# Kernel tuning notes

Measured on AMD Instinct MI355X. Metric: run time of the kernel, lower is better.

Reference implementation:

```python
import jax, jax.numpy as jnp
import numpy as np

N = 10000
E = 640000
IN_CH = 512
OUT_CH = 256
K = 2


def setup_inputs() -> dict:
    key = jax.random.key(0)
    k1, k2, k3, k4, k5 = jax.random.split(key, 5)
    x = jax.random.normal(k1, (N, IN_CH), dtype=jnp.float32)
    edge_index = jax.random.randint(k2, (2, E), 0, N, dtype=jnp.int64)
    lin_w = jax.random.normal(k3, (OUT_CH, IN_CH), dtype=jnp.float32) * (1.0 / np.sqrt(IN_CH))
    lin_b = jax.random.normal(k4, (OUT_CH,), dtype=jnp.float32) * 0.01
    weights = jax.random.uniform(k5, (K,), dtype=jnp.float32)
    return {"x": x, "edge_index": edge_index, "lin_w": lin_w, "lin_b": lin_b, "weights": weights}


def reference(x, edge_index, lin_w, lin_b, weights):
    n = x.shape[0]
    row, col = edge_index[0], edge_index[1]
    # deg = bincount(row); symmetric-normalized edge weights
    deg = jax.ops.segment_sum(jnp.ones(row.shape[0], dtype=x.dtype), row, num_segments=n)
    deg_inv_sqrt = jnp.where(deg > 0, jax.lax.rsqrt(deg), 0.0)
    norm = deg_inv_sqrt[row] * deg_inv_sqrt[col]  # [E]

    def spmm(h):
        # y[i] = sum_{e: row[e]==i} norm[e] * h[col[e]]
        return jax.ops.segment_sum(norm[:, None] * h[col], row, num_segments=n)

    out = x @ lin_w.T + lin_b  # [N, OUT_CH]
    # Faithful ARMA loop: x_k starts from the CURRENT accumulated `out` each hop-group
    for k in range(K):
        x_k = out
        for _ in range(k + 1):
            x_k = spmm(x_k)
        out = out + weights[k] * x_k
    return out
```

## Files before the change

kernel.cpp:

```cpp
#include <hip/hip_runtime.h>

#define N_NODES 10000
#define E_EDGES 640000
#define IN_CH   512
#define OUT_CH  256
#define HALF_CH 128
#define CSR_CAP (E_EDGES + 16 * N_NODES + 128)
#define G_GEMM_X 157
#define G_GEMM  (G_GEMM_X * 2)
#define HBLK    125
#define EPB     5120

typedef short bf16x8 __attribute__((ext_vector_type(8)));
typedef float f32x4  __attribute__((ext_vector_type(4)));

__device__ __forceinline__ unsigned short f2b(float f) {
    unsigned int u = __float_as_uint(f);
    return (unsigned short)((u + 0x7FFFu + ((u >> 16) & 1u)) >> 16);
}
__device__ __forceinline__ float lo16(unsigned int u) { return __uint_as_float(u << 16); }
__device__ __forceinline__ float hi16(unsigned int u) { return __uint_as_float(u & 0xFFFF0000u); }
__device__ __forceinline__ float b2f(unsigned short u) { return __uint_as_float(((unsigned int)u) << 16); }

__global__ __launch_bounds__(256) void hist_rank(const int* __restrict__ row,
                                                 int* __restrict__ cnt,
                                                 unsigned short* __restrict__ rank) {
    __shared__ int hist[N_NODES];
    int b = blockIdx.x, tid = threadIdx.x;
    for (int i = tid; i < N_NODES; i += 256) hist[i] = 0;
    __syncthreads();
    int ebase = b * EPB;
    #pragma unroll 4
    for (int i = tid; i < EPB; i += 256) {
        int r = row[ebase + i];
        rank[ebase + i] = (unsigned short)atomicAdd(&hist[r], 1);
    }
    __syncthreads();
    int* cb = cnt + (size_t)b * N_NODES;
    for (int i = tid; i < N_NODES; i += 256) cb[i] = hist[i];
}

__global__ void alloc2(int* __restrict__ cnt,
                       int2* __restrict__ seg,
                       float* __restrict__ dinv, float* __restrict__ sq,
                       int* __restrict__ counter, int* __restrict__ csr_col, int n) {
    int r = blockIdx.x * blockDim.x + threadIdx.x;
    if (r >= n) return;
    int d = 0;
    for (int b = 0; b < HBLK; b++) d += cnt[(size_t)b * N_NODES + r];
    dinv[r] = (d > 0) ? rsqrtf((float)d) : 0.0f;
    sq[r]   = (d > 0) ? sqrtf((float)d) : 0.0f;
    int pad = (d + 15) & ~15;
    int s = atomicAdd(counter, pad);
    seg[r] = make_int2(s, s + pad);
    int run = s;
    for (int b = 0; b < HBLK; b++) {
        int c = cnt[(size_t)b * N_NODES + r];
        cnt[(size_t)b * N_NODES + r] = run;
        run += c;
    }
    for (int j = d; j < pad; j++) csr_col[s + j] = N_NODES;
}

__global__ __launch_bounds__(256) void gemm_scatter(const float* __restrict__ x,
                                                    const float* __restrict__ w,
                                                    const float* __restrict__ bias,
                                                    const float* __restrict__ dinv,
                                                    unsigned short* __restrict__ h0b,
                                                    const int* __restrict__ row,
                                                    const int* __restrict__ col,
                                                    const int* __restrict__ base,
                                                    const unsigned short* __restrict__ rank,
                                                    int* __restrict__ csr_col) {
    __shared__ unsigned short As[64][72];
    __shared__ unsigned short Bs[128][72];
    int bid = blockIdx.x;
    int tid = threadIdx.x;
    if (bid >= G_GEMM) {
        int sb = bid - G_GEMM;
        const int* bb = base + (size_t)sb * N_NODES;
        int ebase = sb * EPB;
        #pragma unroll 4
        for (int i = tid; i < EPB; i += 256) {
            int e = ebase + i;
            int r = row[e];
            int p = bb[r] + (int)rank[e];
            csr_col[p] = col[e];
        }
        return;
    }
    int bx = bid % G_GEMM_X;
    int plane = bid / G_GEMM_X;
    int wave = tid >> 6, lane = tid & 63, quad = lane >> 4, l16 = lane & 15;
    int row0 = bx * 64;
    int n0 = plane * 128;
    unsigned short* h0b_p = h0b + (size_t)plane * (N_NODES + 1) * HALF_CH;

    int ar = tid >> 2;
    int aseg = (tid & 3) * 16;
    int br = tid >> 1;
    int bseg = (tid & 1) * 32;

    f32x4 acc[8] = {};
    for (int k0 = 0; k0 < IN_CH; k0 += 64) {
        {
            int gr = row0 + ar;
            if (gr < N_NODES) {
                const float4* src = (const float4*)(x + (size_t)gr * IN_CH + k0 + aseg);
                #pragma unroll
                for (int i = 0; i < 4; i++) {
                    float4 v = src[i];
                    ushort4 o;
                    o.x = f2b(v.x); o.y = f2b(v.y); o.z = f2b(v.z); o.w = f2b(v.w);
                    *(ushort4*)&As[ar][aseg + i * 4] = o;
                }
            } else {
                ushort4 z = {0, 0, 0, 0};
                #pragma unroll
                for (int i = 0; i < 4; i++) *(ushort4*)&As[ar][aseg + i * 4] = z;
            }
        }
        {
            const float4* src = (const float4*)(w + (size_t)(n0 + br) * IN_CH + k0 + bseg);
            #pragma unroll
            for (int i = 0; i < 8; i++) {
                float4 v = src[i];
                ushort4 o;
                o.x = f2b(v.x); o.y = f2b(v.y); o.z = f2b(v.z); o.w = f2b(v.w);
                *(ushort4*)&Bs[br][bseg + i * 4] = o;
            }
        }
        __syncthreads();
        #pragma unroll
        for (int kk = 0; kk < 2; kk++) {
            bf16x8 a = *(const bf16x8*)&As[wave * 16 + l16][kk * 32 + quad * 8];
            #pragma unroll
            for (int t = 0; t < 8; t++) {
                bf16x8 b = *(const bf16x8*)&Bs[t * 16 + l16][kk * 32 + quad * 8];
                acc[t] = __builtin_amdgcn_mfma_f32_16x16x32_bf16(a, b, acc[t], 0, 0, 0);
            }
        }
        __syncthreads();
    }
    #pragma unroll
    for (int t = 0; t < 8; t++) {
        int lcol = t * 16 + l16;
        int col_ = n0 + lcol;
        float bv = bias[col_];
        #pragma unroll
        for (int r = 0; r < 4; r++) {
            int grow = row0 + wave * 16 + quad * 4 + r;
            if (grow < N_NODES) {
                float v = acc[t][r] + bv;
                h0b_p[(size_t)grow * HALF_CH + lcol] = f2b(v * dinv[grow]);
            }
        }
    }
    if (bx == 0 && tid < 64)
        ((unsigned int*)(h0b_p + (size_t)N_NODES * HALF_CH))[tid] = 0u;
}

__global__ __launch_bounds__(256) void spmm_kernel(const unsigned short* __restrict__ hb,
                                                   const int2* __restrict__ seg,
                                                   const int* __restrict__ csr_col,
                                                   const float* __restrict__ dinv,
                                                   const float* __restrict__ sq,
                                                   const unsigned short* __restrict__ prev_b,
                                                   const float* __restrict__ wts, int widx,
                                                   unsigned short* __restrict__ yb_out,
                                                   float* __restrict__ axpy_out,
                                                   unsigned short* __restrict__ axpyb_out,
                                                   int n) {
    int plane = blockIdx.x & 1;
    int node = (blockIdx.x >> 1) * 4 + (threadIdx.x >> 6);
    int lane = threadIdx.x & 63;
    if (node >= n) return;
    int sub = lane >> 4, l16 = lane & 15;
    size_t pstride = (size_t)(n + 1) * HALF_CH;
    const unsigned short* hp = hb + (size_t)plane * pstride;

    int2 se = seg[node];
    int s = se.x, e = se.y;
    float acc[8] = {0.f, 0.f, 0.f, 0.f, 0.f, 0.f, 0.f, 0.f};
    if (s < e) {
        int c0 = csr_col[s + 0  + sub];
        int c1 = csr_col[s + 4  + sub];
        int c2 = csr_col[s + 8  + sub];
        int c3 = csr_col[s + 12 + sub];
        int p = s;
        while (true) {
            int pn = p + 16;
            int n0c = csr_col[pn + 0  + sub];
            int n1c = csr_col[pn + 4  + sub];
            int n2c = csr_col[pn + 8  + sub];
            int n3c = csr_col[pn + 12 + sub];
            uint4 v0 = *(const uint4*)(hp + (size_t)c0 * HALF_CH + l16 * 8);
            uint4 v1 = *(const uint4*)(hp + (size_t)c1 * HALF_CH + l16 * 8);
            uint4 v2 = *(const uint4*)(hp + (size_t)c2 * HALF_CH + l16 * 8);
            uint4 v3 = *(const uint4*)(hp + (size_t)c3 * HALF_CH + l16 * 8);
            acc[0] += lo16(v0.x) + lo16(v1.x) + lo16(v2.x) + lo16(v3.x);
            acc[1] += hi16(v0.x) + hi16(v1.x) + hi16(v2.x) + hi16(v3.x);
            acc[2] += lo16(v0.y) + lo16(v1.y) + lo16(v2.y) + lo16(v3.y);
            acc[3] += hi16(v0.y) + hi16(v1.y) + hi16(v2.y) + hi16(v3.y);
            acc[4] += lo16(v0.z) + lo16(v1.z) + lo16(v2.z) + lo16(v3.z);
            acc[5] += hi16(v0.z) + hi16(v1.z) + hi16(v2.z) + hi16(v3.z);
            acc[6] += lo16(v0.w) + lo16(v1.w) + lo16(v2.w) + lo16(v3.w);
            acc[7] += hi16(v0.w) + hi16(v1.w) + hi16(v2.w) + hi16(v3.w);
            c0 = n0c; c1 = n1c; c2 = n2c; c3 = n3c; p = pn;
            if (p >= e) break;
        }
    }
    #pragma unroll
    for (int k = 0; k < 8; k++) {
        acc[k] += __shfl_xor(acc[k], 16, 64);
        acc[k] += __shfl_xor(acc[k], 32, 64);
    }
    if (sub != 0) return;

    float di = dinv[node];
    float y[8];
    #pragma unroll
    for (int k = 0; k < 8; k++) y[k] = di * acc[k];

    size_t pbase = (size_t)plane * pstride + (size_t)node * HALF_CH + l16 * 8;
    size_t padrow = (size_t)plane * pstride + (size_t)n * HALF_CH + l16 * 8;
    if (yb_out) {
        ushort4 o0, o1;
        o0.x = f2b(di * y[0]); o0.y = f2b(di * y[1]); o0.z = f2b(di * y[2]); o0.w = f2b(di * y[3]);
        o1.x = f2b(di * y[4]); o1.y = f2b(di * y[5]); o1.z = f2b(di * y[6]); o1.w = f2b(di * y[7]);
        *(ushort4*)(yb_out + pbase) = o0;
        *(ushort4*)(yb_out + pbase + 4) = o1;
        if (node == 0) {
            ushort4 z = {0, 0, 0, 0};
            *(ushort4*)(yb_out + padrow) = z;
            *(ushort4*)(yb_out + padrow + 4) = z;
        }
    }
    if (prev_b) {
        float wk = wts[widx];
        float sqn = sq[node];
        ushort4 p0 = *(const ushort4*)(prev_b + pbase);
        ushort4 p1 = *(const ushort4*)(prev_b + pbase + 4);
        float o[8];
        o[0] = b2f(p0.x) * sqn + wk * y[0];
        o[1] = b2f(p0.y) * sqn + wk * y[1];
        o[2] = b2f(p0.z) * sqn + wk * y[2];
        o[3] = b2f(p0.w) * sqn + wk * y[3];
        o[4] = b2f(p1.x) * sqn + wk * y[4];
        o[5] = b2f(p1.y) * sqn + wk * y[5];
        o[6] = b2f(p1.z) * sqn + wk * y[6];
        o[7] = b2f(p1.w) * sqn + wk * y[7];
        if (axpy_out) {
            size_t fbase = (size_t)node * OUT_CH + plane * HALF_CH + l16 * 8;
            float4 f0 = {o[0], o[1], o[2], o[3]};
            float4 f1 = {o[4], o[5], o[6], o[7]};
            *(float4*)(axpy_out + fbase) = f0;
            *(float4*)(axpy_out + fbase + 4) = f1;
        }
        if (axpyb_out) {
            ushort4 b0, b1;
            b0.x = f2b(di * o[0]); b0.y = f2b(di * o[1]); b0.z = f2b(di * o[2]); b0.w = f2b(di * o[3]);
            b1.x = f2b(di * o[4]); b1.y = f2b(di * o[5]); b1.z = f2b(di * o[6]); b1.w = f2b(di * o[7]);
            *(ushort4*)(axpyb_out + pbase) = b0;
            *(ushort4*)(axpyb_out + pbase + 4) = b1;
            if (node == 0) {
                ushort4 z = {0, 0, 0, 0};
                *(ushort4*)(axpyb_out + padrow) = z;
                *(ushort4*)(axpyb_out + padrow + 4) = z;
            }
        }
    }
}

extern "C" void kernel_launch(void* const* d_in, const int* in_sizes, int n_in,
                              void* d_out, int out_size, void* d_ws, size_t ws_size,
                              hipStream_t stream) {
    const float* x     = (const float*)d_in[0];
    const int*   ei    = (const int*)d_in[1];
    const float* lin_w = (const float*)d_in[2];
    const float* lin_b = (const float*)d_in[3];
    const float* wts   = (const float*)d_in[4];
    float* out = (float*)d_out;

    char* ws = (char*)d_ws;
    size_t off = 0;
    auto alloc = [&](size_t bytes) -> void* {
        void* p = ws + off;
        off += (bytes + 255) & ~(size_t)255;
        return p;
    };
    int*   cnt      = (int*)  alloc((size_t)HBLK * N_NODES * 4);
    unsigned short* rank = (unsigned short*)alloc((size_t)E_EDGES * 2);
    int*   counter  = (int*)  alloc(256);
    int2*  seg      = (int2*) alloc((size_t)N_NODES * 8);
    float* dinv     = (float*)alloc(N_NODES * 4);
    float* sq       = (float*)alloc(N_NODES * 4);
    int*   csr_col  = (int*)  alloc((size_t)CSR_CAP * 4);
    unsigned short* h0b   = (unsigned short*)alloc((size_t)2 * (N_NODES + 1) * HALF_CH * 2);
    unsigned short* out1b = (unsigned short*)alloc((size_t)2 * (N_NODES + 1) * HALF_CH * 2);
    unsigned short* t2b   = (unsigned short*)alloc((size_t)2 * (N_NODES + 1) * HALF_CH * 2);

    hipMemsetAsync(counter, 0, 4, stream);

    const int* row = ei;
    const int* col = ei + E_EDGES;

    hist_rank<<<HBLK, 256, 0, stream>>>(row, cnt, rank);
    alloc2<<<(N_NODES + 255) / 256, 256, 0, stream>>>(cnt, seg, dinv, sq,
                                                      counter, csr_col, N_NODES);

    gemm_scatter<<<G_GEMM + HBLK, 256, 0, stream>>>(x, lin_w, lin_b, dinv, h0b,
                                                    row, col, cnt, rank, csr_col);

    int sgrid = 2 * ((N_NODES + 3) / 4);
    spmm_kernel<<<sgrid, 256, 0, stream>>>(h0b, seg, csr_col, dinv, sq, h0b,
                                           wts, 0, nullptr, nullptr, out1b, N_NODES);
    spmm_kernel<<<sgrid, 256, 0, stream>>>(out1b, seg, csr_col, dinv, sq, nullptr,
                                           wts, 0, t2b, nullptr, nullptr, N_NODES);
    spmm_kernel<<<sgrid, 256, 0, stream>>>(t2b, seg, csr_col, dinv, sq, out1b,
                                           wts, 1, nullptr, out, nullptr, N_NODES);
}
```

Baseline: 200.2 us.

## Transpose histogram count layout, parallelize CSR allocation per wave, widen SpMM gather unroll

Histogram counts are stored node-major (node × 128 blocks) instead of block-major, so the allocation kernel gives one wave per node and computes the per-block offsets with a wave-level prefix scan instead of a serial 125-iteration loop per thread. CSR segment padding goes from 16 to 32 entries, and the SpMM inner loop gathers 8 neighbor rows per lane per iteration instead of 4, giving more memory-level parallelism. The cost is more padded dummy edges, which are wasted gathers for low-degree nodes, higher register pressure, and strided scattered stores in hist_rank.

```diff
diff --git a/kernel.cpp b/kernel.cpp
--- a/kernel.cpp
+++ b/kernel.cpp
@@ -5,11 +5,12 @@
 #define IN_CH   512
 #define OUT_CH  256
 #define HALF_CH 128
-#define CSR_CAP (E_EDGES + 16 * N_NODES + 128)
+#define CSR_CAP (E_EDGES + 32 * N_NODES + 256)
 #define G_GEMM_X 157
 #define G_GEMM  (G_GEMM_X * 2)
 #define HBLK    125
 #define EPB     5120
+#define CNT_LD  128
 
 typedef short bf16x8 __attribute__((ext_vector_type(8)));
 typedef float f32x4  __attribute__((ext_vector_type(4)));
@@ -36,30 +37,42 @@
         rank[ebase + i] = (unsigned short)atomicAdd(&hist[r], 1);
     }
     __syncthreads();
-    int* cb = cnt + (size_t)b * N_NODES;
-    for (int i = tid; i < N_NODES; i += 256) cb[i] = hist[i];
-}
-
-__global__ void alloc2(int* __restrict__ cnt,
-                       int2* __restrict__ seg,
-                       float* __restrict__ dinv, float* __restrict__ sq,
-                       int* __restrict__ counter, int* __restrict__ csr_col, int n) {
-    int r = blockIdx.x * blockDim.x + threadIdx.x;
+    for (int i = tid; i < N_NODES; i += 256) cnt[(size_t)i * CNT_LD + b] = hist[i];
+}
+
+__global__ __launch_bounds__(256) void alloc2(int* __restrict__ cnt,
+                                              int2* __restrict__ seg,
+                                              float* __restrict__ dinv, float* __restrict__ sq,
+                                              int* __restrict__ counter,
+                                              int* __restrict__ csr_col, int n) {
+    int r = blockIdx.x * 4 + (threadIdx.x >> 6);
+    int lane = threadIdx.x & 63;
     if (r >= n) return;
-    int d = 0;
-    for (int b = 0; b < HBLK; b++) d += cnt[(size_t)b * N_NODES + r];
-    dinv[r] = (d > 0) ? rsqrtf((float)d) : 0.0f;
-    sq[r]   = (d > 0) ? sqrtf((float)d) : 0.0f;
-    int pad = (d + 15) & ~15;
-    int s = atomicAdd(counter, pad);
-    seg[r] = make_int2(s, s + pad);
-    int run = s;
-    for (int b = 0; b < HBLK; b++) {
-        int c = cnt[(size_t)b * N_NODES + r];
-        cnt[(size_t)b * N_NODES + r] = run;
-        run += c;
-    }
-    for (int j = d; j < pad; j++) csr_col[s + j] = N_NODES;
+    int* cr = cnt + (size_t)r * CNT_LD;
+    int v0 = cr[lane];
+    int v1 = (lane < HBLK - 64) ? cr[64 + lane] : 0;
+    int s0 = v0, s1 = v1;
+    #pragma unroll
+    for (int off = 1; off < 64; off <<= 1) {
+        int t0 = __shfl_up(s0, off, 64);
+        int t1 = __shfl_up(s1, off, 64);
+        if (lane >= off) { s0 += t0; s1 += t1; }
+    }
+    int tot0 = __shfl(s0, 63, 64);
+    int d = tot0 + __shfl(s1, 63, 64);
+    int pad = (d + 31) & ~31;
+    int s = 0;
+    if (lane == 0) s = atomicAdd(counter, pad);
+    s = __shfl(s, 0, 64);
+    if (lane == 0) {
+        dinv[r] = (d > 0) ? rsqrtf((float)d) : 0.0f;
+        sq[r]   = (d > 0) ? sqrtf((float)d) : 0.0f;
+        seg[r] = make_int2(s, s + pad);
+    }
+    cr[lane] = s + s0 - v0;
+    if (lane < HBLK - 64) cr[64 + lane] = s + tot0 + s1 - v1;
+    int j = d + lane;
+    if (j < pad) csr_col[s + j] = N_NODES;
 }
 
 __global__ __launch_bounds__(256) void gemm_scatter(const float* __restrict__ x,
@@ -78,13 +91,12 @@
     int tid = threadIdx.x;
     if (bid >= G_GEMM) {
         int sb = bid - G_GEMM;
-        const int* bb = base + (size_t)sb * N_NODES;
         int ebase = sb * EPB;
         #pragma unroll 4
         for (int i = tid; i < EPB; i += 256) {
             int e = ebase + i;
             int r = row[e];
-            int p = bb[r] + (int)rank[e];
+            int p = base[(size_t)r * CNT_LD + sb] + (int)rank[e];
             csr_col[p] = col[e];
         }
         return;
@@ -183,30 +195,29 @@
     int s = se.x, e = se.y;
     float acc[8] = {0.f, 0.f, 0.f, 0.f, 0.f, 0.f, 0.f, 0.f};
     if (s < e) {
-        int c0 = csr_col[s + 0  + sub];
-        int c1 = csr_col[s + 4  + sub];
-        int c2 = csr_col[s + 8  + sub];
-        int c3 = csr_col[s + 12 + sub];
+        int c[8];
+        #pragma unroll
+        for (int g = 0; g < 8; g++) c[g] = csr_col[s + 4 * g + sub];
         int p = s;
         while (true) {
-            int pn = p + 16;
-            int n0c = csr_col[pn + 0  + sub];
-            int n1c = csr_col[pn + 4  + sub];
-            int n2c = csr_col[pn + 8  + sub];
-            int n3c = csr_col[pn + 12 + sub];
-            uint4 v0 = *(const uint4*)(hp + (size_t)c0 * HALF_CH + l16 * 8);
-            uint4 v1 = *(const uint4*)(hp + (size_t)c1 * HALF_CH + l16 * 8);
-            uint4 v2 = *(const uint4*)(hp + (size_t)c2 * HALF_CH + l16 * 8);
-            uint4 v3 = *(const uint4*)(hp + (size_t)c3 * HALF_CH + l16 * 8);
-            acc[0] += lo16(v0.x) + lo16(v1.x) + lo16(v2.x) + lo16(v3.x);
-            acc[1] += hi16(v0.x) + hi16(v1.x) + hi16(v2.x) + hi16(v3.x);
-            acc[2] += lo16(v0.y) + lo16(v1.y) + lo16(v2.y) + lo16(v3.y);
-            acc[3] += hi16(v0.y) + hi16(v1.y) + hi16(v2.y) + hi16(v3.y);
-            acc[4] += lo16(v0.z) + lo16(v1.z) + lo16(v2.z) + lo16(v3.z);
-            acc[5] += hi16(v0.z) + hi16(v1.z) + hi16(v2.z) + hi16(v3.z);
-            acc[6] += lo16(v0.w) + lo16(v1.w) + lo16(v2.w) + lo16(v3.w);
-            acc[7] += hi16(v0.w) + hi16(v1.w) + hi16(v2.w) + hi16(v3.w);
-            c0 = n0c; c1 = n1c; c2 = n2c; c3 = n3c; p = pn;
+            int pn = p + 32;
+            int nc[8];
+            #pragma unroll
+            for (int g = 0; g < 8; g++) nc[g] = csr_col[pn + 4 * g + sub];
+            uint4 v[8];
+            #pragma unroll
+            for (int g = 0; g < 8; g++)
+                v[g] = *(const uint4*)(hp + (size_t)c[g] * HALF_CH + l16 * 8);
+            #pragma unroll
+            for (int g = 0; g < 8; g++) {
+                acc[0] += lo16(v[g].x); acc[1] += hi16(v[g].x);
+                acc[2] += lo16(v[g].y); acc[3] += hi16(v[g].y);
+                acc[4] += lo16(v[g].z); acc[5] += hi16(v[g].z);
+                acc[6] += lo16(v[g].w); acc[7] += hi16(v[g].w);
+            }
+            #pragma unroll
+            for (int g = 0; g < 8; g++) c[g] = nc[g];
+            p = pn;
             if (p >= e) break;
         }
     }
@@ -289,7 +300,7 @@
         off += (bytes + 255) & ~(size_t)255;
         return p;
     };
-    int*   cnt      = (int*)  alloc((size_t)HBLK * N_NODES * 4);
+    int*   cnt      = (int*)  alloc((size_t)N_NODES * CNT_LD * 4);
     unsigned short* rank = (unsigned short*)alloc((size_t)E_EDGES * 2);
     int*   counter  = (int*)  alloc(256);
     int2*  seg      = (int2*) alloc((size_t)N_NODES * 8);
@@ -306,8 +317,8 @@
     const int* col = ei + E_EDGES;
 
     hist_rank<<<HBLK, 256, 0, stream>>>(row, cnt, rank);
-    alloc2<<<(N_NODES + 255) / 256, 256, 0, stream>>>(cnt, seg, dinv, sq,
-                                                      counter, csr_col, N_NODES);
+    alloc2<<<(N_NODES + 3) / 4, 256, 0, stream>>>(cnt, seg, dinv, sq,
+                                                  counter, csr_col, N_NODES);
 
     gemm_scatter<<<G_GEMM + HBLK, 256, 0, stream>>>(x, lin_w, lin_b, dinv, h0b,
                                                     row, col, cnt, rank, csr_col);
```

After: 324.0 us. 1.62x slower.

## Transpose count matrix and parallelize CSR allocation with wave scans

Applied to the files above, without the earlier changes.

Stores per-block row counts as row-major [node][block] with a padded stride so each node's counts are contiguous. The serial per-thread loop over 125 blocks in the allocator is replaced by a wave-level shuffle prefix scan, one node per wave. The global atomic counter is replaced by a single-block exclusive scan over padded degrees. This gives a deterministic, sorted row layout, at the cost of two extra kernel launches and strided writes in the histogram kernel.

```diff
diff --git a/kernel.cpp b/kernel.cpp
--- a/kernel.cpp
+++ b/kernel.cpp
@@ -10,6 +10,7 @@
 #define G_GEMM  (G_GEMM_X * 2)
 #define HBLK    125
 #define EPB     5120
+#define CNT_LD  128
 
 typedef short bf16x8 __attribute__((ext_vector_type(8)));
 typedef float f32x4  __attribute__((ext_vector_type(4)));
@@ -36,30 +37,81 @@
         rank[ebase + i] = (unsigned short)atomicAdd(&hist[r], 1);
     }
     __syncthreads();
-    int* cb = cnt + (size_t)b * N_NODES;
-    for (int i = tid; i < N_NODES; i += 256) cb[i] = hist[i];
-}
-
-__global__ void alloc2(int* __restrict__ cnt,
-                       int2* __restrict__ seg,
-                       float* __restrict__ dinv, float* __restrict__ sq,
-                       int* __restrict__ counter, int* __restrict__ csr_col, int n) {
-    int r = blockIdx.x * blockDim.x + threadIdx.x;
+    for (int i = tid; i < N_NODES; i += 256) cnt[(size_t)i * CNT_LD + b] = hist[i];
+}
+
+__global__ __launch_bounds__(256) void alloc_a(int* __restrict__ cnt,
+                                               int2* __restrict__ pd,
+                                               float* __restrict__ dinv, float* __restrict__ sq,
+                                               int* __restrict__ pads, int n) {
+    int r = blockIdx.x * 4 + (threadIdx.x >> 6);
+    int lane = threadIdx.x & 63;
     if (r >= n) return;
-    int d = 0;
-    for (int b = 0; b < HBLK; b++) d += cnt[(size_t)b * N_NODES + r];
-    dinv[r] = (d > 0) ? rsqrtf((float)d) : 0.0f;
-    sq[r]   = (d > 0) ? sqrtf((float)d) : 0.0f;
+    int* cr = cnt + (size_t)r * CNT_LD;
+    int v0 = cr[lane];
+    int v1 = (lane < HBLK - 64) ? cr[64 + lane] : 0;
+    int s0 = v0, s1 = v1;
+    #pragma unroll
+    for (int off = 1; off < 64; off <<= 1) {
+        int t0 = __shfl_up(s0, off, 64);
+        int t1 = __shfl_up(s1, off, 64);
+        if (lane >= off) { s0 += t0; s1 += t1; }
+    }
+    int tot0 = __shfl(s0, 63, 64);
+    int d = tot0 + __shfl(s1, 63, 64);
     int pad = (d + 15) & ~15;
-    int s = atomicAdd(counter, pad);
-    seg[r] = make_int2(s, s + pad);
-    int run = s;
-    for (int b = 0; b < HBLK; b++) {
-        int c = cnt[(size_t)b * N_NODES + r];
-        cnt[(size_t)b * N_NODES + r] = run;
-        run += c;
-    }
-    for (int j = d; j < pad; j++) csr_col[s + j] = N_NODES;
+    cr[lane] = s0 - v0;
+    if (lane < HBLK - 64) cr[64 + lane] = tot0 + s1 - v1;
+    if (lane == 0) {
+        dinv[r] = (d > 0) ? rsqrtf((float)d) : 0.0f;
+        sq[r]   = (d > 0) ? sqrtf((float)d) : 0.0f;
+        pd[r] = make_int2(d, pad);
+        pads[r] = pad;
+    }
+}
+
+__global__ __launch_bounds__(1024) void scan_pads(const int* __restrict__ pads,
+                                                  int* __restrict__ rowstart, int n) {
+    __shared__ int ls[1024];
+    int t = threadIdx.x;
+    int base = t * 10;
+    int loc[10];
+    int sum = 0;
+    if (base < n) {
+        #pragma unroll
+        for (int i = 0; i < 10; i++) { loc[i] = pads[base + i]; sum += loc[i]; }
+    }
+    ls[t] = sum;
+    __syncthreads();
+    for (int off = 1; off < 1024; off <<= 1) {
+        int v = (t >= off) ? ls[t - off] : 0;
+        __syncthreads();
+        ls[t] += v;
+        __syncthreads();
+    }
+    if (base < n) {
+        int run = ls[t] - sum;
+        #pragma unroll
+        for (int i = 0; i < 10; i++) { rowstart[base + i] = run; run += loc[i]; }
+    }
+}
+
+__global__ __launch_bounds__(256) void alloc_b(int* __restrict__ cnt,
+                                               const int* __restrict__ rowstart,
+                                               const int2* __restrict__ pd,
+                                               int2* __restrict__ seg,
+                                               int* __restrict__ csr_col, int n) {
+    int r = blockIdx.x * 4 + (threadIdx.x >> 6);
+    int lane = threadIdx.x & 63;
+    if (r >= n) return;
+    int s = rowstart[r];
+    int2 pd_ = pd[r];
+    int* cr = cnt + (size_t)r * CNT_LD;
+    cr[lane] += s;
+    if (lane < HBLK - 64) cr[64 + lane] += s;
+    if (lane == 0) seg[r] = make_int2(s, s + pd_.y);
+    int j = pd_.x + lane;
+    if (j < pd_.y) csr_col[s + j] = N_NODES;
 }
 
 __global__ __launch_bounds__(256) void gemm_scatter(const float* __restrict__ x,
@@ -78,13 +130,12 @@
     int tid = threadIdx.x;
     if (bid >= G_GEMM) {
         int sb = bid - G_GEMM;
-        const int* bb = base + (size_t)sb * N_NODES;
         int ebase = sb * EPB;
         #pragma unroll 4
         for (int i = tid; i < EPB; i += 256) {
             int e = ebase + i;
             int r = row[e];
-            int p = bb[r] + (int)rank[e];
+            int p = base[(size_t)r * CNT_LD + sb] + (int)rank[e];
             csr_col[p] = col[e];
         }
         return;
@@ -289,9 +340,11 @@
         off += (bytes + 255) & ~(size_t)255;
         return p;
     };
-    int*   cnt      = (int*)  alloc((size_t)HBLK * N_NODES * 4);
+    int*   cnt      = (int*)  alloc((size_t)N_NODES * CNT_LD * 4);
     unsigned short* rank = (unsigned short*)alloc((size_t)E_EDGES * 2);
-    int*   counter  = (int*)  alloc(256);
+    int2*  pd       = (int2*) alloc((size_t)N_NODES * 8);
+    int*   pads     = (int*)  alloc((size_t)N_NODES * 4);
+    int*   rowstart = (int*)  alloc((size_t)N_NODES * 4);
     int2*  seg      = (int2*) alloc((size_t)N_NODES * 8);
     float* dinv     = (float*)alloc(N_NODES * 4);
     float* sq       = (float*)alloc(N_NODES * 4);
@@ -300,14 +353,13 @@
     unsigned short* out1b = (unsigned short*)alloc((size_t)2 * (N_NODES + 1) * HALF_CH * 2);
     unsigned short* t2b   = (unsigned short*)alloc((size_t)2 * (N_NODES + 1) * HALF_CH * 2);
 
-    hipMemsetAsync(counter, 0, 4, stream);
-
     const int* row = ei;
     const int* col = ei + E_EDGES;
 
     hist_rank<<<HBLK, 256, 0, stream>>>(row, cnt, rank);
-    alloc2<<<(N_NODES + 255) / 256, 256, 0, stream>>>(cnt, seg, dinv, sq,
-                                                      counter, csr_col, N_NODES);
+    alloc_a<<<(N_NODES + 3) / 4, 256, 0, stream>>>(cnt, pd, dinv, sq, pads, N_NODES);
+    scan_pads<<<1, 1024, 0, stream>>>(pads, rowstart, N_NODES);
+    alloc_b<<<(N_NODES + 3) / 4, 256, 0, stream>>>(cnt, rowstart, pd, seg, csr_col, N_NODES);
 
     gemm_scatter<<<G_GEMM + HBLK, 256, 0, stream>>>(x, lin_w, lin_b, dinv, h0b,
                                                     row, col, cnt, rank, csr_col);
```

After: 206.6 us. 3.2% more time.
